# Optimization experiments

Measured on AMD Instinct MI355X. Metric: run time of the kernel, lower is better.

## Reference

```python
import jax, jax.numpy as jnp
import numpy as np
from math import sqrt

N = 40000      # nodes
E = 640000     # edges
DIN = 128
H = 128
DOUT = 128
L = 3          # n_layers
TAU = 1.0
MIN_NORM = 1e-15
BN_EPS = 1e-5


def _norm(v):
    return jnp.linalg.norm(v, axis=-1, keepdims=True)


def reflect_at_zero(x, mu):
    # a = reflection_center(mu); isometric_transform(x, a)
    a = mu / jnp.maximum(jnp.sum(mu * mu, -1, keepdims=True), MIN_NORM)
    r2 = jnp.sum(a * a, -1, keepdims=True) - 1.0
    u = x - a
    return r2 / jnp.maximum(jnp.sum(u * u, -1, keepdims=True), MIN_NORM) * u + a


def reflect_through_zero(p, q, x):
    p_ = p / jnp.maximum(_norm(p), MIN_NORM)
    q_ = q / jnp.maximum(_norm(q), MIN_NORM)
    r = q_ - p_
    m = jnp.sum(r * x, -1, keepdims=True) / jnp.sum(r * r, -1, keepdims=True)
    return x - 2.0 * r * m


def logmap0(y):
    yn = jnp.maximum(_norm(y), MIN_NORM)
    return y / yn * jnp.arctanh(jnp.clip(yn, -1.0 + 1e-15, 1.0 - 1e-15))


def gin_layer(x, src, dst, w1, b1, g, bt, w2, b2):
    # GINConv(eps=0, sum aggregation): mlp(x + sum_{j->i} x_j)
    agg = jax.ops.segment_sum(x[src], dst, num_segments=N)  # [N,H]
    h = x + agg
    h = jax.nn.relu(h @ w1.T + b1)
    mu = jnp.mean(h, axis=0)
    var = jnp.mean((h - mu) ** 2, axis=0)  # biased var (BatchNorm training stats)
    h = (h - mu) / jnp.sqrt(var + BN_EPS) * g + bt
    h = jax.nn.relu(h @ w2.T + b2)
    return h


def setup_inputs() -> dict:
    key = jax.random.key(0)
    ks = jax.random.split(key, 16)
    s = 0.05
    x = jax.random.normal(ks[0], (N, DIN), jnp.float32)
    edge_index = jax.random.randint(ks[1], (2, E), 0, N, dtype=jnp.int64)
    fc0_w = jax.random.normal(ks[2], (H, DIN), jnp.float32) * s
    fc0_b = jax.random.normal(ks[3], (H,), jnp.float32) * s
    w1 = jax.random.normal(ks[4], (L, H, H), jnp.float32) * s
    b1 = jax.random.normal(ks[5], (L, H), jnp.float32) * s
    gamma = jnp.ones((L, H), jnp.float32)
    beta = jnp.zeros((L, H), jnp.float32)
    w2 = jax.random.normal(ks[6], (L, H, H), jnp.float32) * s
    b2 = jax.random.normal(ks[7], (L, H), jnp.float32) * s
    fc_out_w = jax.random.normal(ks[8], (DOUT, H), jnp.float32) * s
    fc_out_b = jax.random.normal(ks[9], (DOUT,), jnp.float32) * s
    p = (-1.0 / sqrt(H)) * jnp.ones((H,), jnp.float32)
    return {"x": x, "edge_index": edge_index, "fc0_w": fc0_w, "fc0_b": fc0_b,
            "w1": w1, "b1": b1, "gamma": gamma, "beta": beta, "w2": w2, "b2": b2,
            "fc_out_w": fc_out_w, "fc_out_b": fc_out_b, "p": p}


def reference(x, edge_index, fc0_w, fc0_b, w1, b1, gamma, beta, w2, b2, fc_out_w, fc_out_b, p):
    # With continuous random features every row is unique, so torch.unique(dim=0)
    # is a pure permutation (counts==1) and the unique/scatter_add/gather pipeline
    # collapses to per-node tree embeddings; the final index_select undoes the perm.
    scaling = jnp.tanh(jnp.asarray(TAU, jnp.float32) / 2.0)
    src, dst = edge_index[0], edge_index[1]
    h = jax.nn.relu(x @ fc0_w.T + fc0_b)                 # [N,H]
    hd = jax.lax.stop_gradient(h)                        # unique under no_grad
    z_prev = jnp.zeros((N, H), h.dtype)                  # level-0 root embedding
    z_cur = scaling * hd / _norm(hd)                     # level-1 embedding
    for i in range(L):
        h = gin_layer(h, src, dst, w1[i], b1[i], gamma[i], beta[i], w2[i], b2[i])
        hd = jax.lax.stop_gradient(h)
        z_ch = scaling * hd / _norm(hd)
        z_par = reflect_at_zero(z_prev, z_cur)
        z_ch = reflect_through_zero(z_par, p, z_ch)
        z_all = reflect_at_zero(z_ch, z_cur)
        z_prev, z_cur = z_cur, z_all
    xh = logmap0(z_cur)                                  # [N,H] tangent space
    out = xh @ fc_out_w.T + fc_out_b                     # [N,DOUT]
    return out / jnp.maximum(_norm(out), 1e-12)          # F.normalize
```

## Files before the change

kernel.cpp:

```cpp
#include <hip/hip_runtime.h>
#include <math.h>

#define NN 40000
#define HD 128
#define NE 640000
#define MINN 1e-15f
#define NSB 157
#define GB  2500
#define HB_BLK 512

typedef __attribute__((ext_vector_type(8))) short bf16x8;
typedef __attribute__((ext_vector_type(4))) float f32x4;

__device__ __forceinline__ float red16(float v){
  v += __shfl_xor(v, 1, 64); v += __shfl_xor(v, 2, 64);
  v += __shfl_xor(v, 4, 64); v += __shfl_xor(v, 8, 64);
  return v;
}

__device__ __forceinline__ float bf2f(short h){
  return __uint_as_float(((unsigned)(unsigned short)h) << 16);
}
__device__ __forceinline__ short f2bf(float v){
  unsigned u = __float_as_uint(v);
  u += 0x7FFF + ((u >> 16) & 1);
  return (short)(u >> 16);
}

#define GACC(A,V) \
  A[0] += __uint_as_float((V).x << 16); A[1] += __uint_as_float((V).x & 0xffff0000u); \
  A[2] += __uint_as_float((V).y << 16); A[3] += __uint_as_float((V).y & 0xffff0000u); \
  A[4] += __uint_as_float((V).z << 16); A[5] += __uint_as_float((V).z & 0xffff0000u); \
  A[6] += __uint_as_float((V).w << 16); A[7] += __uint_as_float((V).w & 0xffff0000u);

__device__ __forceinline__ void loadA_g(const float* __restrict__ A, long rb,
                                        int l15, int kg, float av[4][8]){
  #pragma unroll
  for (int ks = 0; ks < 4; ++ks){
    const float* ap = A + (rb + l15)*HD + ks*32 + kg*8;
    float4 a0 = *(const float4*)ap;
    float4 a1 = *(const float4*)(ap + 4);
    av[ks][0]=a0.x; av[ks][1]=a0.y; av[ks][2]=a0.z; av[ks][3]=a0.w;
    av[ks][4]=a1.x; av[ks][5]=a1.y; av[ks][6]=a1.z; av[ks][7]=a1.w;
  }
}

__device__ __forceinline__ void mfma_core(const float av[4][8],
    const bf16x8* __restrict__ bh, const bf16x8* __restrict__ bl,
    int lane, f32x4 acc[8]){
  #pragma unroll
  for (int ct = 0; ct < 8; ++ct){
    acc[ct][0]=0.f; acc[ct][1]=0.f; acc[ct][2]=0.f; acc[ct][3]=0.f;
  }
  #pragma unroll
  for (int ks = 0; ks < 4; ++ks){
    bf16x8 ah, al;
    #pragma unroll
    for (int j = 0; j < 8; ++j){
      float v = av[ks][j];
      short hh = f2bf(v);
      short ll = f2bf(v - bf2f(hh));
      ah[j] = hh; al[j] = ll;
    }
    #pragma unroll
    for (int ct = 0; ct < 8; ++ct){
      bf16x8 bhv = bh[(ks*8 + ct)*64 + lane];
      bf16x8 blv = bl[(ks*8 + ct)*64 + lane];
      acc[ct] = __builtin_amdgcn_mfma_f32_16x16x32_bf16(ah, bhv, acc[ct], 0, 0, 0);
      acc[ct] = __builtin_amdgcn_mfma_f32_16x16x32_bf16(al, bhv, acc[ct], 0, 0, 0);
      acc[ct] = __builtin_amdgcn_mfma_f32_16x16x32_bf16(ah, blv, acc[ct], 0, 0, 0);
    }
  }
}

__device__ __forceinline__ void biasrelu(f32x4 acc[8], const float* __restrict__ bias,
                                         int l15, bool relu){
  #pragma unroll
  for (int ct = 0; ct < 8; ++ct){
    float bb = bias[ct*16 + l15];
    #pragma unroll
    for (int q = 0; q < 4; ++q){
      float v = acc[ct][q] + bb;
      if (relu) v = fmaxf(v, 0.f);
      acc[ct][q] = v;
    }
  }
}

__global__ __launch_bounds__(64) void zero_prep_k(const float* __restrict__ fc0_w,
    const float* __restrict__ w1, const float* __restrict__ w2,
    const float* __restrict__ fco_w, bf16x8* __restrict__ bhi,
    bf16x8* __restrict__ blo, int* __restrict__ cnt, float* __restrict__ part2){
  int bid = blockIdx.x;
  if (bid < 256){
    int gid = bid*64 + threadIdx.x;
    int widx = gid >> 11;
    const float* W;
    if (widx == 0)      W = fc0_w;
    else if (widx <= 3) W = w1 + (size_t)(widx-1)*HD*HD;
    else if (widx <= 6) W = w2 + (size_t)(widx-4)*HD*HD;
    else                W = fco_w;
    int f  = gid & 2047;
    int ln = f & 63;
    int ct = (f >> 6) & 7;
    int ks = f >> 9;
    int n  = ct*16 + (ln & 15);
    int k0 = ks*32 + (ln >> 4)*8;
    bf16x8 hv, lv;
    #pragma unroll
    for (int j = 0; j < 8; ++j){
      float v = W[n*HD + k0 + j];
      short hh = f2bf(v);
      short ll = f2bf(v - bf2f(hh));
      hv[j] = hh; lv[j] = ll;
    }
    bhi[widx*2048 + f] = hv; blo[widx*2048 + f] = lv;
  } else {
    int i = (bid-256)*64 + threadIdx.x;
    const int st = 161*64;
    for (int j = i; j < NN; j += st) cnt[j] = 0;
    for (int j = i; j < 2048; j += st) part2[j] = 0.f;
  }
}

__global__ __launch_bounds__(64) void fc0hist_k(const float* __restrict__ x,
    const int* __restrict__ dst, int* __restrict__ cnt,
    const bf16x8* __restrict__ bhi, const bf16x8* __restrict__ blo,
    const float* __restrict__ fc0_b, float* __restrict__ h,
    unsigned short* __restrict__ hb, float* __restrict__ zB, float scaling){
  int bid = blockIdx.x;
  if (bid >= GB){
    int i = (bid - GB)*64 + threadIdx.x;
    const int st = HB_BLK*64;
    for (; i < NE; i += st) atomicAdd(&cnt[dst[i]], 1);
    return;
  }
  const int lane = threadIdx.x;
  const int l15 = lane & 15, kg = lane >> 4;
  const long rb = (long)bid*16;
  float av[4][8]; loadA_g(x, rb, l15, kg, av);
  f32x4 acc[8]; mfma_core(av, bhi, blo, lane, acc);
  biasrelu(acc, fc0_b, l15, true);
  #pragma unroll
  for (int ct = 0; ct < 8; ++ct)
    #pragma unroll
    for (int q = 0; q < 4; ++q){
      float v = acc[ct][q];
      long row = rb + kg*4 + q;
      h[row*HD + ct*16 + l15] = v;
      hb[row*HD + ct*16 + l15] = (unsigned short)f2bf(v);
    }
  #pragma unroll
  for (int q = 0; q < 4; ++q){
    float ss = 0.f;
    #pragma unroll
    for (int ct = 0; ct < 8; ++ct) ss = fmaf(acc[ct][q], acc[ct][q], ss);
    ss = red16(ss);
    float sc2 = scaling / sqrtf(ss);
    long row = rb + kg*4 + q;
    #pragma unroll
    for (int ct = 0; ct < 8; ++ct)
      zB[row*HD + ct*16 + l15] = acc[ct][q]*sc2;
  }
}

__global__ __launch_bounds__(256) void scan1_k(const int* __restrict__ cnt,
    int* __restrict__ locpre, int* __restrict__ btot){
  __shared__ int s[256];
  int t = threadIdx.x;
  int idx = blockIdx.x*256 + t;
  int v = (idx < NN) ? cnt[idx] : 0;
  s[t] = v; __syncthreads();
  for (int off = 1; off < 256; off <<= 1){
    int x = (t >= off) ? s[t-off] : 0;
    __syncthreads(); s[t] += x; __syncthreads();
  }
  locpre[idx] = s[t] - v;
  if (t == 255) btot[blockIdx.x] = s[255];
}

__global__ __launch_bounds__(256) void scan23_k(const int* __restrict__ btot,
    const int* __restrict__ locpre, int* __restrict__ ptr, int* __restrict__ fil){
  __shared__ int s[256];
  int t = threadIdx.x;
  int v = (t < NSB) ? btot[t] : 0;
  s[t] = v; __syncthreads();
  for (int off = 1; off < 256; off <<= 1){
    int x = (t >= off) ? s[t-off] : 0;
    __syncthreads(); s[t] += x; __syncthreads();
  }
  int bid = blockIdx.x;
  int pre = (bid == 0) ? 0 : s[bid-1];
  int idx = bid*256 + t;
  if (idx < NN){
    int v2 = pre + locpre[idx];
    ptr[idx] = v2; fil[idx] = v2;
  }
  if (bid == 0 && t == 0) ptr[NN] = s[NSB-1];
}

__global__ void fill_k(const int* __restrict__ src, const int* __restrict__ dst,
    int* __restrict__ fill, unsigned short* __restrict__ eidx, int ne){
  int i = blockIdx.x*blockDim.x + threadIdx.x;
  int st = gridDim.x*blockDim.x;
  for (; i < ne; i += st){
    int d = dst[i];
    int pos = atomicAdd(&fill[d], 1);
    eidx[pos] = (unsigned short)src[i];
  }
}

__global__ __launch_bounds__(256) void gw1_k(const float* __restrict__ h,
    const bf16x8* __restrict__ bhi, const bf16x8* __restrict__ blo,
    const float* __restrict__ bias, float* __restrict__ t,
    float* __restrict__ part2, const uint4* __restrict__ hb4,
    const int* __restrict__ gptr, const unsigned short* __restrict__ eidx)
{
  __shared__ float tl[16*132];
  const int tid = threadIdx.x;
  const int lane = tid & 63;
  const int wv = tid >> 6;
  const int l15 = lane & 15, kg = lane >> 4;
  const long rb = (long)blockIdx.x*16;

  {
    const int r = wv*4 + kg;
    const long node = rb + r;
    int beg = gptr[node], end = gptr[node+1];
    const float4* selfp = (const float4*)(h + node*HD) + l15*2;
    float4 s0 = selfp[0], s1 = selfp[1];
    float ga[8] = {s0.x,s0.y,s0.z,s0.w,s1.x,s1.y,s1.z,s1.w};
    int e = beg;
    for (; e + 8 <= end; e += 8){
      int i0 = eidx[e],   i1 = eidx[e+1], i2 = eidx[e+2], i3 = eidx[e+3];
      int i4 = eidx[e+4], i5 = eidx[e+5], i6 = eidx[e+6], i7 = eidx[e+7];
      uint4 v0 = hb4[(long)i0*16 + l15];
      uint4 v1 = hb4[(long)i1*16 + l15];
      uint4 v2 = hb4[(long)i2*16 + l15];
      uint4 v3 = hb4[(long)i3*16 + l15];
      uint4 v4 = hb4[(long)i4*16 + l15];
      uint4 v5 = hb4[(long)i5*16 + l15];
      uint4 v6 = hb4[(long)i6*16 + l15];
      uint4 v7 = hb4[(long)i7*16 + l15];
      GACC(ga,v0) GACC(ga,v1) GACC(ga,v2) GACC(ga,v3)
      GACC(ga,v4) GACC(ga,v5) GACC(ga,v6) GACC(ga,v7)
    }
    if (e + 4 <= end){
      int i0 = eidx[e], i1 = eidx[e+1], i2 = eidx[e+2], i3 = eidx[e+3];
      uint4 v0 = hb4[(long)i0*16 + l15];
      uint4 v1 = hb4[(long)i1*16 + l15];
      uint4 v2 = hb4[(long)i2*16 + l15];
      uint4 v3 = hb4[(long)i3*16 + l15];
      GACC(ga,v0) GACC(ga,v1) GACC(ga,v2) GACC(ga,v3)
      e += 4;
    }
    for (; e < end; ++e){
      uint4 v = hb4[(long)eidx[e]*16 + l15];
      GACC(ga,v)
    }
    float4* tp = (float4*)(tl + r*132 + l15*8);
    float4 o0 = {ga[0],ga[1],ga[2],ga[3]};
    float4 o1 = {ga[4],ga[5],ga[6],ga[7]};
    tp[0] = o0; tp[1] = o1;
  }
  __syncthreads();
  if (wv != 0) return;

  float av[4][8];
  #pragma unroll
  for (int ks = 0; ks < 4; ++ks){
    const float* ap = tl + l15*132 + ks*32 + kg*8;
    float4 a0 = *(const float4*)ap;
    float4 a1 = *(const float4*)(ap + 4);
    av[ks][0]=a0.x; av[ks][1]=a0.y; av[ks][2]=a0.z; av[ks][3]=a0.w;
    av[ks][4]=a1.x; av[ks][5]=a1.y; av[ks][6]=a1.z; av[ks][7]=a1.w;
  }
  f32x4 acc[8]; mfma_core(av, bhi, blo, lane, acc);
  biasrelu(acc, bias, l15, true);

  #pragma unroll
  for (int ct = 0; ct < 8; ++ct){
    float s = 0.f, q2 = 0.f;
    #pragma unroll
    for (int q = 0; q < 4; ++q){
      float v = acc[ct][q];
      s += v; q2 = fmaf(v, v, q2);
    }
    s  += __shfl_xor(s, 16, 64);  s  += __shfl_xor(s, 32, 64);
    q2 += __shfl_xor(q2, 16, 64); q2 += __shfl_xor(q2, 32, 64);
    if (kg == 0){
      const int slot = (blockIdx.x & 7)*256;
      atomicAdd(&part2[slot + ct*16 + l15], s);
      atomicAdd(&part2[slot + 128 + ct*16 + l15], q2);
    }
  }

  #pragma unroll
  for (int ct = 0; ct < 8; ++ct)
    #pragma unroll
    for (int q = 0; q < 4; ++q)
      t[(rb + kg*4 + q)*HD + ct*16 + l15] = acc[ct][q];
}

template<bool RELU, bool BN_IN, bool XH_IN, bool NORM_OUT,
         bool WRITE_HB, bool WRITE_OUT, bool ZSTEP, bool ZFIRST>
__global__ __launch_bounds__(64) void mgemm_k(const float* __restrict__ A,
    const bf16x8* __restrict__ bhi, const bf16x8* __restrict__ blo,
    const float* __restrict__ bias, const float* __restrict__ scale,
    const float* __restrict__ shift, float* __restrict__ out,
    unsigned short* __restrict__ hbout, float* __restrict__ zout, float scaling,
    const float* __restrict__ zpin, const float* __restrict__ zcin,
    const float* __restrict__ pvec)
{
  const int lane = threadIdx.x;
  const int l15 = lane & 15, kg = lane >> 4;
  const long rb = (long)blockIdx.x*16;

  float av[4][8];
  loadA_g(A, rb, l15, kg, av);

  float zc_a[4][8], zp_a[4][8], pvr[8];
  if constexpr (ZSTEP){
    #pragma unroll
    for (int q = 0; q < 4; ++q){
      const long row = rb + kg*4 + q;
      #pragma unroll
      for (int ct = 0; ct < 8; ++ct)
        zc_a[q][ct] = zcin[row*HD + ct*16 + l15];
    }
    if constexpr (!ZFIRST){
      #pragma unroll
      for (int q = 0; q < 4; ++q){
        const long row = rb + kg*4 + q;
        #pragma unroll
        for (int ct = 0; ct < 8; ++ct)
          zp_a[q][ct] = zpin[row*HD + ct*16 + l15];
      }
    }
    #pragma unroll
    for (int ct = 0; ct < 8; ++ct) pvr[ct] = pvec[ct*16 + l15];
  }

  if (BN_IN){
    #pragma unroll
    for (int ks = 0; ks < 4; ++ks){
      const int k0 = ks*32 + kg*8;
      float4 s0 = *(const float4*)(scale + k0);
      float4 s1 = *(const float4*)(scale + k0 + 4);
      float4 h0 = *(const float4*)(shift + k0);
      float4 h1 = *(const float4*)(shift + k0 + 4);
      float sc[8] = {s0.x,s0.y,s0.z,s0.w,s1.x,s1.y,s1.z,s1.w};
      float sh[8] = {h0.x,h0.y,h0.z,h0.w,h1.x,h1.y,h1.z,h1.w};
      #pragma unroll
      for (int j = 0; j < 8; ++j)
        av[ks][j] = fmaf(av[ks][j], sc[j], sh[j]);
    }
  }
  if (XH_IN){
    float ss = 0.f;
    #pragma unroll
    for (int ks = 0; ks < 4; ++ks)
      #pragma unroll
      for (int j = 0; j < 8; ++j)
        ss = fmaf(av[ks][j], av[ks][j], ss);
    ss += __shfl_xor(ss, 16, 64);
    ss += __shfl_xor(ss, 32, 64);
    float n = sqrtf(ss);
    float yn = fmaxf(n, MINN);
    float c = fminf(yn, 1.0f);
    float at = 0.5f*logf((1.0f + c)/(1.0f - c));
    float scx = at / yn;
    #pragma unroll
    for (int ks = 0; ks < 4; ++ks)
      #pragma unroll
      for (int j = 0; j < 8; ++j)
        av[ks][j] *= scx;
  }

  f32x4 acc[8];
  mfma_core(av, bhi, blo, lane, acc);
  biasrelu(acc, bias, l15, RELU);

  if (NORM_OUT){
    float ss[4] = {0.f,0.f,0.f,0.f};
    #pragma unroll
    for (int ct = 0; ct < 8; ++ct)
      #pragma unroll
      for (int q = 0; q < 4; ++q)
        ss[q] = fmaf(acc[ct][q], acc[ct][q], ss[q]);
    #pragma unroll
    for (int q = 0; q < 4; ++q){
      #pragma unroll
      for (int m = 1; m < 16; m <<= 1) ss[q] += __shfl_xor(ss[q], m, 64);
      ss[q] = 1.0f / fmaxf(sqrtf(ss[q]), 1e-12f);
    }
    #pragma unroll
    for (int ct = 0; ct < 8; ++ct)
      #pragma unroll
      for (int q = 0; q < 4; ++q)
        acc[ct][q] *= ss[q];
  }

  if constexpr (ZSTEP){
    float pq = 0.f;
    #pragma unroll
    for (int ct = 0; ct < 8; ++ct) pq = fmaf(pvr[ct], pvr[ct], pq);
    pq = red16(pq);
    float qi = 1.0f / fmaxf(sqrtf(pq), MINN);
    #pragma unroll
    for (int ct = 0; ct < 8; ++ct) pvr[ct] *= qi;

    #pragma unroll
    for (int q = 0; q < 4; ++q){
      const long row = rb + kg*4 + q;
      float zc[8], zp[8];
      #pragma unroll
      for (int ct = 0; ct < 8; ++ct) zc[ct] = zc_a[q][ct];
      if constexpr (!ZFIRST){
        #pragma unroll
        for (int ct = 0; ct < 8; ++ct) zp[ct] = zp_a[q][ct];
      } else {
        #pragma unroll
        for (int ct = 0; ct < 8; ++ct) zp[ct] = 0.f;
      }
      float hh = 0.f, cc = 0.f;
      #pragma unroll
      for (int ct = 0; ct < 8; ++ct){
        hh = fmaf(acc[ct][q], acc[ct][q], hh);
        cc = fmaf(zc[ct], zc[ct], cc);
      }
      hh = red16(hh); cc = red16(cc);
      float zs = scaling / sqrtf(hh);
      float di = 1.0f / fmaxf(cc, MINN);
      float r2 = cc*di*di - 1.0f;
      float a[8], u[8]; float uu = 0.f;
      #pragma unroll
      for (int ct = 0; ct < 8; ++ct){
        a[ct] = zc[ct]*di;
        u[ct] = zp[ct] - a[ct];
        uu = fmaf(u[ct], u[ct], uu);
      }
      uu = red16(uu);
      float f = r2 / fmaxf(uu, MINN);
      float zpar[8]; float pn2 = 0.f;
      #pragma unroll
      for (int ct = 0; ct < 8; ++ct){
        zpar[ct] = fmaf(f, u[ct], a[ct]);
        pn2 = fmaf(zpar[ct], zpar[ct], pn2);
      }
      pn2 = red16(pn2);
      float pinv = 1.0f / fmaxf(sqrtf(pn2), MINN);
      float rv[8], zch[8]; float rz = 0.f, rr = 0.f;
      #pragma unroll
      for (int ct = 0; ct < 8; ++ct){
        zch[ct] = acc[ct][q]*zs;
        rv[ct] = pvr[ct] - zpar[ct]*pinv;
        rz = fmaf(rv[ct], zch[ct], rz);
        rr = fmaf(rv[ct], rv[ct], rr);
      }
      rz = red16(rz); rr = red16(rr);
      float mm = rz / rr;
      float u2[8]; float uu2 = 0.f;
      #pragma unroll
      for (int ct = 0; ct < 8; ++ct){
        float z2 = fmaf(-2.0f*mm, rv[ct], zch[ct]);
        u2[ct] = z2 - a[ct];
        uu2 = fmaf(u2[ct], u2[ct], uu2);
      }
      uu2 = red16(uu2);
      float f2 = r2 / fmaxf(uu2, MINN);
      #pragma unroll
      for (int ct = 0; ct < 8; ++ct)
        zout[row*HD + ct*16 + l15] = fmaf(f2, u2[ct], a[ct]);
    }
  }

  if constexpr (WRITE_OUT || WRITE_HB){
    #pragma unroll
    for (int ct = 0; ct < 8; ++ct)
      #pragma unroll
      for (int q = 0; q < 4; ++q){
        float v = acc[ct][q];
        long row = rb + kg*4 + q;
        if (WRITE_OUT) out[row*HD + ct*16 + l15] = v;
        if (WRITE_HB) hbout[row*HD + ct*16 + l15] = (unsigned short)f2bf(v);
      }
  }
}

__global__ __launch_bounds__(256) void bnfin_k(float* __restrict__ part2,
    const float* __restrict__ g, const float* __restrict__ b,
    float* __restrict__ scale, float* __restrict__ shift){
  __shared__ float sm[256];
  float tot = 0.f;
  #pragma unroll
  for (int r = 0; r < 8; ++r) tot += part2[r*256 + threadIdx.x];
  sm[threadIdx.x] = tot;
  __syncthreads();
  if (threadIdx.x < 128){
    int c = threadIdx.x;
    float s = sm[c], q = sm[c + 128];
    float mu  = s * (1.0f/NN);
    float var = q * (1.0f/NN) - mu*mu;
    float istd = rsqrtf(var + 1e-5f);
    float scv = g[c]*istd;
    scale[c] = scv;
    shift[c] = fmaf(-mu, scv, b[c]);
  }
  #pragma unroll
  for (int r = 0; r < 8; ++r) part2[r*256 + threadIdx.x] = 0.f;
}

extern "C" void kernel_launch(void* const* d_in, const int* in_sizes, int n_in,
                              void* d_out, int out_size, void* d_ws, size_t ws_size,
                              hipStream_t stream) {
  const float* x       = (const float*)d_in[0];
  const int*   ei      = (const int*)  d_in[1];
  const float* fc0_w   = (const float*)d_in[2];
  const float* fc0_b   = (const float*)d_in[3];
  const float* w1      = (const float*)d_in[4];
  const float* b1      = (const float*)d_in[5];
  const float* gamma   = (const float*)d_in[6];
  const float* beta    = (const float*)d_in[7];
  const float* w2      = (const float*)d_in[8];
  const float* b2      = (const float*)d_in[9];
  const float* fco_w   = (const float*)d_in[10];
  const float* fco_b   = (const float*)d_in[11];
  const float* p       = (const float*)d_in[12];

  float* out = (float*)d_out;
  float* ws  = (float*)d_ws;

  float* h     = ws;
  float* zA    = h   + (size_t)NN*HD;
  float* zB    = zA  + (size_t)NN*HD;
  float* part2 = zB  + (size_t)NN*HD;
  float* scale = part2 + 8*256;
  float* shift = scale + 128;
  bf16x8* bhi  = (bf16x8*)(shift + 128);
  bf16x8* blo  = bhi + 8*2048;
  unsigned short* hb = (unsigned short*)(blo + 8*2048);
  int* cnt     = (int*)(hb + (size_t)NN*HD);
  int* ptr     = cnt + NN;
  int* fil     = ptr + NN + 1;
  unsigned short* eidx = (unsigned short*)(fil + NN);
  int* locpre  = (int*)(eidx + NE);
  int* btot    = locpre + NSB*256;
  float* t = out;

  const int* src = ei;
  const int* dst = ei + NE;
  const float scaling = tanhf(0.5f);

  zero_prep_k<<<417, 64, 0, stream>>>(fc0_w, w1, w2, fco_w, bhi, blo, cnt, part2);

  fc0hist_k<<<GB + HB_BLK, 64, 0, stream>>>(x, dst, cnt, bhi, blo, fc0_b,
                                            h, hb, zB, scaling);

  scan1_k<<<NSB, 256, 0, stream>>>(cnt, locpre, btot);
  scan23_k<<<NSB, 256, 0, stream>>>(btot, locpre, ptr, fil);
  fill_k<<<512, 256, 0, stream>>>(src, dst, fil, eidx, NE);

  float* zprev = zA; float* zcur = zB;

  for (int i = 0; i < 3; ++i) {
    gw1_k<<<GB, 256, 0, stream>>>(
        h, bhi + (1+i)*2048, blo + (1+i)*2048, b1 + i*HD, t, part2,
        (const uint4*)hb, ptr, eidx);
    bnfin_k<<<1, 256, 0, stream>>>(part2, gamma + i*HD, beta + i*HD, scale, shift);
    if (i == 0)
      mgemm_k<true,true,false,false,true,true,true,true>
          <<<GB, 64, 0, stream>>>(
          t, bhi + 4*2048, blo + 4*2048, b2, scale, shift, h, hb,
          zprev, scaling, zprev, zcur, p);
    else if (i == 1)
      mgemm_k<true,true,false,false,true,true,true,false>
          <<<GB, 64, 0, stream>>>(
          t, bhi + 5*2048, blo + 5*2048, b2 + HD, scale, shift, h, hb,
          zprev, scaling, zprev, zcur, p);
    else
      mgemm_k<true,true,false,false,false,false,true,false>
          <<<GB, 64, 0, stream>>>(
          t, bhi + 6*2048, blo + 6*2048, b2 + 2*HD, scale, shift, h, nullptr,
          zprev, scaling, zprev, zcur, p);
    float* tmp = zprev; zprev = zcur; zcur = tmp;
  }

  mgemm_k<false,false,true,true,false,true,false,false>
      <<<GB, 64, 0, stream>>>(
      zcur, bhi + 7*2048, blo + 7*2048, fco_b, nullptr, nullptr, out,
      nullptr, nullptr, 0.f, nullptr, nullptr, nullptr);
}
```

Baseline: 294.2 us.

## Split neighbor aggregation across two thread halves and fuse scan kernels

The gather-aggregate phase of gw1_k now uses 512 threads, with each node's edge list split between two 16-thread groups. The two partial sums go to separate shared-memory tiles and are added when loaded for the MFMA. This doubles memory-level parallelism for the irregular gather. The two-pass prefix scan is also merged into one kernel, where each block recomputes its prefix by summing all earlier counts, dropping a launch at the cost of redundant reads. The larger blocks add shared memory and idle threads during the GEMM phase, which may reduce occupancy.

```diff
diff --git a/kernel.cpp b/kernel.cpp
--- a/kernel.cpp
+++ b/kernel.cpp
@@ -164,39 +164,32 @@
   }
 }
 
-__global__ __launch_bounds__(256) void scan1_k(const int* __restrict__ cnt,
-    int* __restrict__ locpre, int* __restrict__ btot){
+__global__ __launch_bounds__(256) void scanall_k(const int* __restrict__ cnt,
+    int* __restrict__ ptr, int* __restrict__ fil){
   __shared__ int s[256];
-  int t = threadIdx.x;
-  int idx = blockIdx.x*256 + t;
+  const int b = blockIdx.x, t = threadIdx.x;
+  const int lim = b*256;
+  int acc = 0;
+  for (int i = t; i < lim; i += 256) acc += cnt[i];
+  s[t] = acc; __syncthreads();
+  for (int off = 128; off; off >>= 1){
+    if (t < off) s[t] += s[t+off];
+    __syncthreads();
+  }
+  const int pre = s[0];
+  __syncthreads();
+  const int idx = lim + t;
   int v = (idx < NN) ? cnt[idx] : 0;
   s[t] = v; __syncthreads();
   for (int off = 1; off < 256; off <<= 1){
     int x = (t >= off) ? s[t-off] : 0;
     __syncthreads(); s[t] += x; __syncthreads();
   }
-  locpre[idx] = s[t] - v;
-  if (t == 255) btot[blockIdx.x] = s[255];
-}
-
-__global__ __launch_bounds__(256) void scan23_k(const int* __restrict__ btot,
-    const int* __restrict__ locpre, int* __restrict__ ptr, int* __restrict__ fil){
-  __shared__ int s[256];
-  int t = threadIdx.x;
-  int v = (t < NSB) ? btot[t] : 0;
-  s[t] = v; __syncthreads();
-  for (int off = 1; off < 256; off <<= 1){
-    int x = (t >= off) ? s[t-off] : 0;
-    __syncthreads(); s[t] += x; __syncthreads();
-  }
-  int bid = blockIdx.x;
-  int pre = (bid == 0) ? 0 : s[bid-1];
-  int idx = bid*256 + t;
   if (idx < NN){
-    int v2 = pre + locpre[idx];
+    int v2 = pre + s[t] - v;
     ptr[idx] = v2; fil[idx] = v2;
   }
-  if (bid == 0 && t == 0) ptr[NN] = s[NSB-1];
+  if (b == NSB-1 && t == 255) ptr[NN] = pre + s[255];
 }
 
 __global__ void fill_k(const int* __restrict__ src, const int* __restrict__ dst,
@@ -210,13 +203,13 @@
   }
 }
 
-__global__ __launch_bounds__(256) void gw1_k(const float* __restrict__ h,
+__global__ __launch_bounds__(512) void gw1_k(const float* __restrict__ h,
     const bf16x8* __restrict__ bhi, const bf16x8* __restrict__ blo,
     const float* __restrict__ bias, float* __restrict__ t,
     float* __restrict__ part2, const uint4* __restrict__ hb4,
     const int* __restrict__ gptr, const unsigned short* __restrict__ eidx)
 {
-  __shared__ float tl[16*132];
+  __shared__ float tl[2*16*132];
   const int tid = threadIdx.x;
   const int lane = tid & 63;
   const int wv = tid >> 6;
@@ -224,41 +217,50 @@
   const long rb = (long)blockIdx.x*16;
 
   {
-    const int r = wv*4 + kg;
+    const int g = tid >> 4;
+    const int r = g & 15;
+    const int half = g >> 4;
+    const int l = tid & 15;
     const long node = rb + r;
     int beg = gptr[node], end = gptr[node+1];
-    const float4* selfp = (const float4*)(h + node*HD) + l15*2;
-    float4 s0 = selfp[0], s1 = selfp[1];
-    float ga[8] = {s0.x,s0.y,s0.z,s0.w,s1.x,s1.y,s1.z,s1.w};
-    int e = beg;
-    for (; e + 8 <= end; e += 8){
+    int mid = beg + ((end - beg) >> 1);
+    int e  = half ? mid : beg;
+    int e1 = half ? end : mid;
+    float ga[8] = {0.f,0.f,0.f,0.f,0.f,0.f,0.f,0.f};
+    if (!half){
+      const float4* selfp = (const float4*)(h + node*HD) + l*2;
+      float4 s0 = selfp[0], s1 = selfp[1];
+      ga[0]=s0.x; ga[1]=s0.y; ga[2]=s0.z; ga[3]=s0.w;
+      ga[4]=s1.x; ga[5]=s1.y; ga[6]=s1.z; ga[7]=s1.w;
+    }
+    for (; e + 8 <= e1; e += 8){
       int i0 = eidx[e],   i1 = eidx[e+1], i2 = eidx[e+2], i3 = eidx[e+3];
       int i4 = eidx[e+4], i5 = eidx[e+5], i6 = eidx[e+6], i7 = eidx[e+7];
-      uint4 v0 = hb4[(long)i0*16 + l15];
-      uint4 v1 = hb4[(long)i1*16 + l15];
-      uint4 v2 = hb4[(long)i2*16 + l15];
-      uint4 v3 = hb4[(long)i3*16 + l15];
-      uint4 v4 = hb4[(long)i4*16 + l15];
-      uint4 v5 = hb4[(long)i5*16 + l15];
-      uint4 v6 = hb4[(long)i6*16 + l15];
-      uint4 v7 = hb4[(long)i7*16 + l15];
+      uint4 v0 = hb4[(long)i0*16 + l];
+      uint4 v1 = hb4[(long)i1*16 + l];
+      uint4 v2 = hb4[(long)i2*16 + l];
+      uint4 v3 = hb4[(long)i3*16 + l];
+      uint4 v4 = hb4[(long)i4*16 + l];
+      uint4 v5 = hb4[(long)i5*16 + l];
+      uint4 v6 = hb4[(long)i6*16 + l];
+      uint4 v7 = hb4[(long)i7*16 + l];
       GACC(ga,v0) GACC(ga,v1) GACC(ga,v2) GACC(ga,v3)
       GACC(ga,v4) GACC(ga,v5) GACC(ga,v6) GACC(ga,v7)
     }
-    if (e + 4 <= end){
+    if (e + 4 <= e1){
       int i0 = eidx[e], i1 = eidx[e+1], i2 = eidx[e+2], i3 = eidx[e+3];
-      uint4 v0 = hb4[(long)i0*16 + l15];
-      uint4 v1 = hb4[(long)i1*16 + l15];
-      uint4 v2 = hb4[(long)i2*16 + l15];
-      uint4 v3 = hb4[(long)i3*16 + l15];
+      uint4 v0 = hb4[(long)i0*16 + l];
+      uint4 v1 = hb4[(long)i1*16 + l];
+      uint4 v2 = hb4[(long)i2*16 + l];
+      uint4 v3 = hb4[(long)i3*16 + l];
       GACC(ga,v0) GACC(ga,v1) GACC(ga,v2) GACC(ga,v3)
       e += 4;
     }
-    for (; e < end; ++e){
-      uint4 v = hb4[(long)eidx[e]*16 + l15];
+    for (; e < e1; ++e){
+      uint4 v = hb4[(long)eidx[e]*16 + l];
       GACC(ga,v)
     }
-    float4* tp = (float4*)(tl + r*132 + l15*8);
+    float4* tp = (float4*)(tl + half*2112 + r*132 + l*8);
     float4 o0 = {ga[0],ga[1],ga[2],ga[3]};
     float4 o1 = {ga[4],ga[5],ga[6],ga[7]};
     tp[0] = o0; tp[1] = o1;
@@ -272,8 +274,10 @@
     const float* ap = tl + l15*132 + ks*32 + kg*8;
     float4 a0 = *(const float4*)ap;
     float4 a1 = *(const float4*)(ap + 4);
-    av[ks][0]=a0.x; av[ks][1]=a0.y; av[ks][2]=a0.z; av[ks][3]=a0.w;
-    av[ks][4]=a1.x; av[ks][5]=a1.y; av[ks][6]=a1.z; av[ks][7]=a1.w;
+    float4 b0 = *(const float4*)(ap + 2112);
+    float4 b1 = *(const float4*)(ap + 2112 + 4);
+    av[ks][0]=a0.x+b0.x; av[ks][1]=a0.y+b0.y; av[ks][2]=a0.z+b0.z; av[ks][3]=a0.w+b0.w;
+    av[ks][4]=a1.x+b1.x; av[ks][5]=a1.y+b1.y; av[ks][6]=a1.z+b1.z; av[ks][7]=a1.w+b1.w;
   }
   f32x4 acc[8]; mfma_core(av, bhi, blo, lane, acc);
   biasrelu(acc, bias, l15, true);
@@ -544,8 +548,6 @@
   int* ptr     = cnt + NN;
   int* fil     = ptr + NN + 1;
   unsigned short* eidx = (unsigned short*)(fil + NN);
-  int* locpre  = (int*)(eidx + NE);
-  int* btot    = locpre + NSB*256;
   float* t = out;
 
   const int* src = ei;
@@ -557,14 +559,13 @@
   fc0hist_k<<<GB + HB_BLK, 64, 0, stream>>>(x, dst, cnt, bhi, blo, fc0_b,
                                             h, hb, zB, scaling);
 
-  scan1_k<<<NSB, 256, 0, stream>>>(cnt, locpre, btot);
-  scan23_k<<<NSB, 256, 0, stream>>>(btot, locpre, ptr, fil);
+  scanall_k<<<NSB, 256, 0, stream>>>(cnt, ptr, fil);
   fill_k<<<512, 256, 0, stream>>>(src, dst, fil, eidx, NE);
 
   float* zprev = zA; float* zcur = zB;
 
   for (int i = 0; i < 3; ++i) {
-    gw1_k<<<GB, 256, 0, stream>>>(
+    gw1_k<<<GB, 512, 0, stream>>>(
         h, bhi + (1+i)*2048, blo + (1+i)*2048, b1 + i*HD, t, part2,
         (const uint4*)hb, ptr, eidx);
     bnfin_k<<<1, 256, 0, stream>>>(part2, gamma + i*HD, beta + i*HD, scale, shift);
```

Result: slower. 317.8 us (+8.0%).
